# Performance work log

Hardware: AMD Instinct MI355X
Metric: run time of the kernel (lower is better)

Reference implementation:

```python
import jax, jax.numpy as jnp
import numpy as np

GRID_MIN = -2.0
GRID_MAX = 2.0
NUM_GRIDS = 8
IN_DIM = 512
OUT_DIM = 512
N = 16384
SPLINE_SCALE = 0.1


def setup_inputs() -> dict:
    key = jax.random.key(0)
    k_x, k_sw, k_w, k_b = jax.random.split(key, 4)
    x = jax.random.normal(k_x, (N, IN_DIM), dtype=jnp.float32)
    grid = jnp.linspace(GRID_MIN, GRID_MAX, NUM_GRIDS, dtype=jnp.float32)
    spline_weight = jax.random.normal(k_sw, (IN_DIM * NUM_GRIDS, OUT_DIM), dtype=jnp.float32) * SPLINE_SCALE
    bound = 1.0 / np.sqrt(IN_DIM)
    base_w = jax.random.uniform(k_w, (OUT_DIM, IN_DIM), minval=-bound, maxval=bound, dtype=jnp.float32)
    base_b = jax.random.uniform(k_b, (OUT_DIM,), minval=-bound, maxval=bound, dtype=jnp.float32)
    return {"x": x, "grid": grid, "spline_weight": spline_weight, "base_w": base_w, "base_b": base_b}


def reference(x, grid, spline_weight, base_w, base_b):
    # Gaussian RBF basis over the grid: (N, in_dim, num_grids)
    h = (GRID_MAX - GRID_MIN) / (NUM_GRIDS - 1)  # grid spacing
    basis = jnp.exp(-(((x[..., None] - grid) / h) ** 2))
    ret = basis.reshape(x.shape[0], -1) @ spline_weight  # (N, out_dim)
    base = jax.nn.silu(x) @ base_w.T + base_b
    return ret + base
```

## Files before the change

### kernel.cpp

```cpp
#include <hip/hip_runtime.h>
#include <hip/hip_bf16.h>

typedef __attribute__((ext_vector_type(8))) short short8;
typedef __attribute__((ext_vector_type(4))) float floatx4;

#define N_ROWS   16384
#define IN_DIM   512
#define OUT_DIM  512
#define K_SPLINE 4096
#define K_TOT    4608
#define NKT      72
#define NPER     36
#define NSPER    32
#define NKTILE   144
#define L2E      1.4426950408889634f
#define C2E      0.13533528323661270f

__device__ __forceinline__ unsigned short f2bf(float f) {
    unsigned int u = __float_as_uint(f);
    unsigned int r = u + 0x7FFFu + ((u >> 16) & 1u);
    return (unsigned short)(r >> 16);
}

__device__ __forceinline__ unsigned packtrunc(float f0, float f1) {
    return __builtin_amdgcn_perm(__float_as_uint(f1), __float_as_uint(f0), 0x07060302);
}

__global__ __launch_bounds__(256) void prep_kernel(
    const float* __restrict__ sw, const float* __restrict__ bw,
    unsigned short* __restrict__ Btf)
{
    const int t     = threadIdx.x;
    const int lane  = t & 63;
    const int kt32  = blockIdx.x * 4 + (t >> 6);
    const int ct    = blockIdx.y;
    const int mn    = lane & 15, q = lane >> 4;
    const int n     = ct * 16 + mn;
    const int kbase = kt32 * 32 + q * 8;
    short8 v;
    if (kbase < K_SPLINE) {
        #pragma unroll
        for (int j = 0; j < 8; ++j)
            v[j] = (short)f2bf(sw[(size_t)(kbase + j) * OUT_DIM + n]);
    } else {
        #pragma unroll
        for (int j = 0; j < 8; ++j)
            v[j] = (short)f2bf(bw[(size_t)n * IN_DIM + (kbase + j - K_SPLINE)]);
    }
    reinterpret_cast<short8*>(Btf)[(size_t)(ct * NKTILE + kt32) * 64 + lane] = v;
}

__device__ __forceinline__ uint4 basis_pack(float X) {
    const float u = fmaf(1.75f, X, 3.5f);
    float b = __builtin_amdgcn_exp2f(-(u * u) * L2E);
    float r = __builtin_amdgcn_exp2f(fmaf(2.0f * L2E, u, -L2E));
    float v[8];
    v[0] = b;
    #pragma unroll
    for (int j = 1; j < 8; ++j) { b *= r; r *= C2E; v[j] = b; }
    uint4 p;
    p.x = packtrunc(v[0], v[1]);
    p.y = packtrunc(v[2], v[3]);
    p.z = packtrunc(v[4], v[5]);
    p.w = packtrunc(v[6], v[7]);
    return p;
}

__device__ __forceinline__ void stageA128(unsigned short* dst, const float* xrow,
                                          int rowA, int colq, int p, float4 xsp)
{
    unsigned short* arow = dst + rowA * 128;
    if (p < NSPER) {
        const float xv[4] = {xsp.x, xsp.y, xsp.z, xsp.w};
        #pragma unroll
        for (int e = 0; e < 4; ++e) {
            const uint4 pk = basis_pack(xv[e]);
            const int blk = (colq * 4 + e) ^ (rowA & 15);
            *reinterpret_cast<uint4*>(arow + blk * 8) = pk;
        }
    } else {
        const float* xs = xrow + (p - NSPER) * 128 + colq * 32;
        #pragma unroll
        for (int e = 0; e < 4; ++e) {
            const float4 a0 = *reinterpret_cast<const float4*>(xs + e * 8);
            const float4 a1 = *reinterpret_cast<const float4*>(xs + e * 8 + 4);
            const float f[8] = {a0.x, a0.y, a0.z, a0.w, a1.x, a1.y, a1.z, a1.w};
            float s[8];
            #pragma unroll
            for (int j = 0; j < 8; ++j)
                s[j] = f[j] * __builtin_amdgcn_rcpf(
                    1.0f + __builtin_amdgcn_exp2f(-f[j] * L2E));
            uint4 pk;
            pk.x = packtrunc(s[0], s[1]);
            pk.y = packtrunc(s[2], s[3]);
            pk.z = packtrunc(s[4], s[5]);
            pk.w = packtrunc(s[6], s[7]);
            const int blk = (colq * 4 + e) ^ (rowA & 15);
            *reinterpret_cast<uint4*>(arow + blk * 8) = pk;
        }
    }
}

template<bool PREP>
__device__ __forceinline__ void load_bfrags(short8 dst[4][2], const short8* __restrict__ Bf,
                                            const size_t* bbase, int kt,
                                            const float* __restrict__ sw,
                                            const float* __restrict__ bw,
                                            int col0, int lane)
{
    if (kt >= NKT) return;
    if (PREP) {
        #pragma unroll
        for (int nt = 0; nt < 4; ++nt)
            #pragma unroll
            for (int s = 0; s < 2; ++s)
                dst[nt][s] = Bf[bbase[nt] + (size_t)(kt * 2 + s) * 64];
    } else {
        const int mn = lane & 15, q = lane >> 4;
        #pragma unroll
        for (int nt = 0; nt < 4; ++nt) {
            const int n = col0 + nt * 16 + mn;
            #pragma unroll
            for (int s = 0; s < 2; ++s) {
                short8 v;
                #pragma unroll
                for (int j = 0; j < 8; ++j) {
                    const int k = (kt * 2 + s) * 32 + q * 8 + j;
                    const float val = (k < K_SPLINE)
                        ? sw[(size_t)k * OUT_DIM + n]
                        : bw[(size_t)n * IN_DIM + (k - K_SPLINE)];
                    v[j] = (short)f2bf(val);
                }
                dst[nt][s] = v;
            }
        }
    }
}

template<bool PREP>
__global__ __launch_bounds__(256, 2) void kan_kernel(
    const float* __restrict__ x,
    const unsigned short* __restrict__ Btf,
    const float* __restrict__ sw,
    const float* __restrict__ bw,
    const float* __restrict__ bias,
    float* __restrict__ out)
{
    __shared__ unsigned short Als[2][64 * 128];

    const int tid  = threadIdx.x;
    const int wn   = tid >> 6;
    const int lane = tid & 63;
    const int q    = lane >> 4;
    const int mn   = lane & 15;
    const int bid  = blockIdx.x;
    const int row0 = (bid >> 1) * 64;
    const int col0 = (bid & 1) * 256 + wn * 64;

    const int rowA = tid >> 2;
    const int colq = tid & 3;
    const float* xrow = x + (size_t)(row0 + rowA) * IN_DIM;

    size_t bbase[4];
    #pragma unroll
    for (int nt = 0; nt < 4; ++nt)
        bbase[nt] = (size_t)(((col0 >> 4) + nt) * NKTILE) * 64 + lane;
    const short8* Bf = reinterpret_cast<const short8*>(Btf);

    floatx4 acc[4][4];
    #pragma unroll
    for (int i = 0; i < 4; ++i)
        #pragma unroll
        for (int j = 0; j < 4; ++j)
            acc[i][j] = (floatx4){0.f, 0.f, 0.f, 0.f};

    short8 bb[2][4][2];

    float4 xsp = *reinterpret_cast<const float4*>(xrow + colq * 4);
    stageA128(&Als[0][0], xrow, rowA, colq, 0, xsp);
    load_bfrags<PREP>(bb[0], Bf, bbase, 0, sw, bw, col0, lane);
    xsp = *reinterpret_cast<const float4*>(xrow + 16 + colq * 4);
    __syncthreads();

    for (int p = 0; p < NPER; ++p) {
        const unsigned short* Acur = &Als[p & 1][0];
        unsigned short*       Anxt = &Als[(p & 1) ^ 1][0];

        load_bfrags<PREP>(bb[1], Bf, bbase, 2 * p + 1, sw, bw, col0, lane);

        if (p + 1 < NPER) {
            stageA128(Anxt, xrow, rowA, colq, p + 1, xsp);
            if (p + 2 < NSPER)
                xsp = *reinterpret_cast<const float4*>(
                    xrow + (p + 2) * 16 + colq * 4);
        }

        #pragma unroll
        for (int hh = 0; hh < 2; ++hh) {
            #pragma unroll
            for (int s = 0; s < 2; ++s) {
                const int st = hh * 2 + s;
                short8 af[4];
                #pragma unroll
                for (int mt = 0; mt < 4; ++mt) {
                    const int r = mt * 16 + mn;
                    af[mt] = *reinterpret_cast<const short8*>(
                        Acur + r * 128 + (((st * 4 + q) ^ (r & 15)) * 8));
                }
                #pragma unroll
                for (int mt = 0; mt < 4; ++mt)
                    #pragma unroll
                    for (int nt = 0; nt < 4; ++nt)
                        acc[mt][nt] = __builtin_amdgcn_mfma_f32_16x16x32_bf16(
                            af[mt], bb[hh][nt][s], acc[mt][nt], 0, 0, 0);
            }
            if (hh == 0)
                load_bfrags<PREP>(bb[0], Bf, bbase, 2 * p + 2, sw, bw, col0, lane);
        }
        __syncthreads();
    }

    #pragma unroll
    for (int nt = 0; nt < 4; ++nt) {
        const int col = col0 + nt * 16 + mn;
        const float bv = bias[col];
        #pragma unroll
        for (int mt = 0; mt < 4; ++mt) {
            const int rb = row0 + mt * 16 + q * 4;
            #pragma unroll
            for (int e = 0; e < 4; ++e)
                out[(size_t)(rb + e) * OUT_DIM + col] = acc[mt][nt][e] + bv;
        }
    }
}

extern "C" void kernel_launch(void* const* d_in, const int* in_sizes, int n_in,
                              void* d_out, int out_size, void* d_ws, size_t ws_size,
                              hipStream_t stream)
{
    const float* x    = (const float*)d_in[0];
    const float* sw   = (const float*)d_in[2];
    const float* bw   = (const float*)d_in[3];
    const float* bias = (const float*)d_in[4];
    float* out = (float*)d_out;

    const size_t bt_bytes = (size_t)OUT_DIM * K_TOT * sizeof(unsigned short);
    if (ws_size >= bt_bytes) {
        unsigned short* Btf = (unsigned short*)d_ws;
        prep_kernel<<<dim3(NKTILE / 4, OUT_DIM / 16), 256, 0, stream>>>(sw, bw, Btf);
        kan_kernel<true><<<dim3(512), 256, 0, stream>>>(
            x, Btf, sw, bw, bias, out);
    } else {
        kan_kernel<false><<<dim3(512), 256, 0, stream>>>(
            x, nullptr, sw, bw, bias, out);
    }
}
```

Measured before the change: 167.1 us.

## Switch to 32x32x16 MFMA tiles with interleaved staging and software-pipelined A loads

```diff
diff --git a/kernel.cpp b/kernel.cpp
--- a/kernel.cpp
+++ b/kernel.cpp
@@ -1,18 +1,19 @@
 #include <hip/hip_runtime.h>
 #include <hip/hip_bf16.h>
 
-typedef __attribute__((ext_vector_type(8))) short short8;
-typedef __attribute__((ext_vector_type(4))) float floatx4;
+typedef __attribute__((ext_vector_type(8)))  short  short8;
+typedef __attribute__((ext_vector_type(16))) float  floatx16;
 
 #define N_ROWS   16384
 #define IN_DIM   512
 #define OUT_DIM  512
 #define K_SPLINE 4096
 #define K_TOT    4608
-#define NKT      72
+#define NKT16    288
+#define NKT64    72
 #define NPER     36
 #define NSPER    32
-#define NKTILE   144
+#define NCT      16
 #define L2E      1.4426950408889634f
 #define C2E      0.13533528323661270f
 
@@ -30,24 +31,23 @@
     const float* __restrict__ sw, const float* __restrict__ bw,
     unsigned short* __restrict__ Btf)
 {
-    const int t     = threadIdx.x;
-    const int lane  = t & 63;
-    const int kt32  = blockIdx.x * 4 + (t >> 6);
-    const int ct    = blockIdx.y;
-    const int mn    = lane & 15, q = lane >> 4;
-    const int n     = ct * 16 + mn;
-    const int kbase = kt32 * 32 + q * 8;
+    const int t    = threadIdx.x;
+    const int lane = t & 63;
+    const int kt16 = blockIdx.x * 4 + (t >> 6);
+    const int ct   = blockIdx.y;
+    const int n    = ct * 32 + (lane & 31);
+    const int kb   = kt16 * 16 + (lane >> 5) * 8;
     short8 v;
-    if (kbase < K_SPLINE) {
+    if (kb < K_SPLINE) {
         #pragma unroll
         for (int j = 0; j < 8; ++j)
-            v[j] = (short)f2bf(sw[(size_t)(kbase + j) * OUT_DIM + n]);
+            v[j] = (short)f2bf(sw[(size_t)(kb + j) * OUT_DIM + n]);
     } else {
         #pragma unroll
         for (int j = 0; j < 8; ++j)
-            v[j] = (short)f2bf(bw[(size_t)n * IN_DIM + (kbase + j - K_SPLINE)]);
-    }
-    reinterpret_cast<short8*>(Btf)[(size_t)(ct * NKTILE + kt32) * 64 + lane] = v;
+            v[j] = (short)f2bf(bw[(size_t)n * IN_DIM + (kb + j - K_SPLINE)]);
+    }
+    reinterpret_cast<short8*>(Btf)[(size_t)(ct * NKT16 + kt16) * 64 + lane] = v;
 }
 
 __device__ __forceinline__ uint4 basis_pack(float X) {
@@ -66,66 +66,58 @@
     return p;
 }
 
-__device__ __forceinline__ void stageA128(unsigned short* dst, const float* xrow,
-                                          int rowA, int colq, int p, float4 xsp)
-{
-    unsigned short* arow = dst + rowA * 128;
-    if (p < NSPER) {
-        const float xv[4] = {xsp.x, xsp.y, xsp.z, xsp.w};
-        #pragma unroll
-        for (int e = 0; e < 4; ++e) {
-            const uint4 pk = basis_pack(xv[e]);
-            const int blk = (colq * 4 + e) ^ (rowA & 15);
-            *reinterpret_cast<uint4*>(arow + blk * 8) = pk;
-        }
+__device__ __forceinline__ void stage_spl_e(unsigned short* arow, int rowA, int colq,
+                                            float X, int e)
+{
+    const uint4 pk = basis_pack(X);
+    const int blk = (colq * 4 + e) ^ (rowA & 15);
+    *reinterpret_cast<uint4*>(arow + blk * 8) = pk;
+}
+
+__device__ __forceinline__ void stage_silu_e(unsigned short* arow, const float* xs,
+                                             int rowA, int colq, int e)
+{
+    const float4 a0 = *reinterpret_cast<const float4*>(xs + e * 8);
+    const float4 a1 = *reinterpret_cast<const float4*>(xs + e * 8 + 4);
+    const float f[8] = {a0.x, a0.y, a0.z, a0.w, a1.x, a1.y, a1.z, a1.w};
+    float sv[8];
+    #pragma unroll
+    for (int j = 0; j < 8; ++j)
+        sv[j] = f[j] * __builtin_amdgcn_rcpf(
+            1.0f + __builtin_amdgcn_exp2f(-f[j] * L2E));
+    uint4 pk;
+    pk.x = packtrunc(sv[0], sv[1]);
+    pk.y = packtrunc(sv[2], sv[3]);
+    pk.z = packtrunc(sv[4], sv[5]);
+    pk.w = packtrunc(sv[6], sv[7]);
+    const int blk = (colq * 4 + e) ^ (rowA & 15);
+    *reinterpret_cast<uint4*>(arow + blk * 8) = pk;
+}
+
+template<bool PREP>
+__device__ __forceinline__ void load_bhalf(short8 dst[2][4], const short8* __restrict__ Bf,
+                                           const unsigned* boff, int kt64,
+                                           const float* __restrict__ sw,
+                                           const float* __restrict__ bw,
+                                           int col0, int lane)
+{
+    if (PREP) {
+        #pragma unroll
+        for (int nt = 0; nt < 2; ++nt)
+            #pragma unroll
+            for (int s = 0; s < 4; ++s)
+                dst[nt][s] = Bf[boff[nt] + (unsigned)(kt64 * 4 + s) * 64u];
     } else {
-        const float* xs = xrow + (p - NSPER) * 128 + colq * 32;
-        #pragma unroll
-        for (int e = 0; e < 4; ++e) {
-            const float4 a0 = *reinterpret_cast<const float4*>(xs + e * 8);
-            const float4 a1 = *reinterpret_cast<const float4*>(xs + e * 8 + 4);
-            const float f[8] = {a0.x, a0.y, a0.z, a0.w, a1.x, a1.y, a1.z, a1.w};
-            float s[8];
-            #pragma unroll
-            for (int j = 0; j < 8; ++j)
-                s[j] = f[j] * __builtin_amdgcn_rcpf(
-                    1.0f + __builtin_amdgcn_exp2f(-f[j] * L2E));
-            uint4 pk;
-            pk.x = packtrunc(s[0], s[1]);
-            pk.y = packtrunc(s[2], s[3]);
-            pk.z = packtrunc(s[4], s[5]);
-            pk.w = packtrunc(s[6], s[7]);
-            const int blk = (colq * 4 + e) ^ (rowA & 15);
-            *reinterpret_cast<uint4*>(arow + blk * 8) = pk;
-        }
-    }
-}
-
-template<bool PREP>
-__device__ __forceinline__ void load_bfrags(short8 dst[4][2], const short8* __restrict__ Bf,
-                                            const size_t* bbase, int kt,
-                                            const float* __restrict__ sw,
-                                            const float* __restrict__ bw,
-                                            int col0, int lane)
-{
-    if (kt >= NKT) return;
-    if (PREP) {
-        #pragma unroll
-        for (int nt = 0; nt < 4; ++nt)
-            #pragma unroll
-            for (int s = 0; s < 2; ++s)
-                dst[nt][s] = Bf[bbase[nt] + (size_t)(kt * 2 + s) * 64];
-    } else {
-        const int mn = lane & 15, q = lane >> 4;
-        #pragma unroll
-        for (int nt = 0; nt < 4; ++nt) {
-            const int n = col0 + nt * 16 + mn;
-            #pragma unroll
-            for (int s = 0; s < 2; ++s) {
+        #pragma unroll
+        for (int nt = 0; nt < 2; ++nt) {
+            const int n = col0 + nt * 32 + (lane & 31);
+            #pragma unroll
+            for (int s = 0; s < 4; ++s) {
+                const int kb = (kt64 * 4 + s) * 16 + (lane >> 5) * 8;
                 short8 v;
                 #pragma unroll
                 for (int j = 0; j < 8; ++j) {
-                    const int k = (kt * 2 + s) * 32 + q * 8 + j;
+                    const int k = kb + j;
                     const float val = (k < K_SPLINE)
                         ? sw[(size_t)k * OUT_DIM + n]
                         : bw[(size_t)n * IN_DIM + (k - K_SPLINE)];
@@ -135,6 +127,58 @@
             }
         }
     }
+}
+
+template<int MODE, bool PREP>
+__device__ __forceinline__ void period_body(
+    int p,
+    const unsigned short* __restrict__ Acur,
+    unsigned short* __restrict__ anrow,
+    short8 bb[2][2][4], floatx16 acc[2][2],
+    const int aoff[2][8],
+    const unsigned* boff, const short8* __restrict__ Bf,
+    float4& xsp, const float* __restrict__ xrow, int rowA, int colq,
+    const float* __restrict__ sw, const float* __restrict__ bw,
+    int col0, int lane)
+{
+    const float xv[4] = {xsp.x, xsp.y, xsp.z, xsp.w};
+    const float* xs = (MODE == 1) ? (xrow + (p + 1 - NSPER) * 128 + colq * 32)
+                                  : xrow;
+
+    short8 af[2][2];
+    #pragma unroll
+    for (int mt = 0; mt < 2; ++mt)
+        af[0][mt] = *reinterpret_cast<const short8*>(Acur + aoff[mt][0]);
+
+    #pragma unroll
+    for (int st = 0; st < 8; ++st) {
+        const int hh = st >> 2, s = st & 3, cb = st & 1;
+        if (st < 7) {
+            #pragma unroll
+            for (int mt = 0; mt < 2; ++mt)
+                af[cb ^ 1][mt] = *reinterpret_cast<const short8*>(
+                    Acur + aoff[mt][st + 1]);
+        }
+        if (MODE == 0 && st < 4) stage_spl_e(anrow, rowA, colq, xv[st], st);
+        if (MODE == 1 && st < 4) stage_silu_e(anrow, xs, rowA, colq, st);
+        if (st == 0)
+            load_bhalf<PREP>(bb[1], Bf, boff, 2 * p + 1, sw, bw, col0, lane);
+        if (MODE != 2 && st == 4)
+            load_bhalf<PREP>(bb[0], Bf, boff, 2 * p + 2, sw, bw, col0, lane);
+        if (MODE == 0 && st == 3) {
+            const int pp = (p + 2 < NSPER) ? p + 2 : NSPER - 1;
+            xsp = *reinterpret_cast<const float4*>(xrow + pp * 16 + colq * 4);
+        }
+        __builtin_amdgcn_s_setprio(1);
+        #pragma unroll
+        for (int mt = 0; mt < 2; ++mt)
+            #pragma unroll
+            for (int nt = 0; nt < 2; ++nt)
+                acc[mt][nt] = __builtin_amdgcn_mfma_f32_32x32x16_bf16(
+                    af[cb][mt], bb[hh][nt][s], acc[mt][nt], 0, 0, 0);
+        __builtin_amdgcn_s_setprio(0);
+    }
+    __syncthreads();
 }
 
 template<bool PREP>
@@ -151,8 +195,8 @@
     const int tid  = threadIdx.x;
     const int wn   = tid >> 6;
     const int lane = tid & 63;
-    const int q    = lane >> 4;
-    const int mn   = lane & 15;
+    const int h    = lane >> 5;
+    const int mn   = lane & 31;
     const int bid  = blockIdx.x;
     const int row0 = (bid >> 1) * 64;
     const int col0 = (bid & 1) * 256 + wn * 64;
@@ -161,75 +205,72 @@
     const int colq = tid & 3;
     const float* xrow = x + (size_t)(row0 + rowA) * IN_DIM;
 
-    size_t bbase[4];
-    #pragma unroll
-    for (int nt = 0; nt < 4; ++nt)
-        bbase[nt] = (size_t)(((col0 >> 4) + nt) * NKTILE) * 64 + lane;
+    unsigned boff[2];
+    #pragma unroll
+    for (int nt = 0; nt < 2; ++nt)
+        boff[nt] = (unsigned)(((col0 >> 5) + nt) * NKT16) * 64u + (unsigned)lane;
     const short8* Bf = reinterpret_cast<const short8*>(Btf);
 
-    floatx4 acc[4][4];
-    #pragma unroll
-    for (int i = 0; i < 4; ++i)
-        #pragma unroll
-        for (int j = 0; j < 4; ++j)
-            acc[i][j] = (floatx4){0.f, 0.f, 0.f, 0.f};
-
-    short8 bb[2][4][2];
+    int aoff[2][8];
+    #pragma unroll
+    for (int mt = 0; mt < 2; ++mt) {
+        const int r = mt * 32 + mn;
+        #pragma unroll
+        for (int st = 0; st < 8; ++st)
+            aoff[mt][st] = r * 128 + (((st * 2 + h) ^ (r & 15)) * 8);
+    }
+
+    floatx16 acc[2][2];
+    #pragma unroll
+    for (int i = 0; i < 2; ++i)
+        #pragma unroll
+        for (int j = 0; j < 2; ++j)
+            #pragma unroll
+            for (int e = 0; e < 16; ++e)
+                acc[i][j][e] = 0.f;
+
+    short8 bb[2][2][4];
 
     float4 xsp = *reinterpret_cast<const float4*>(xrow + colq * 4);
-    stageA128(&Als[0][0], xrow, rowA, colq, 0, xsp);
-    load_bfrags<PREP>(bb[0], Bf, bbase, 0, sw, bw, col0, lane);
+    {
+        unsigned short* arow0 = &Als[0][0] + rowA * 128;
+        const float xv0[4] = {xsp.x, xsp.y, xsp.z, xsp.w};
+        #pragma unroll
+        for (int e = 0; e < 4; ++e)
+            stage_spl_e(arow0, rowA, colq, xv0[e], e);
+    }
+    load_bhalf<PREP>(bb[0], Bf, boff, 0, sw, bw, col0, lane);
     xsp = *reinterpret_cast<const float4*>(xrow + 16 + colq * 4);
     __syncthreads();
 
-    for (int p = 0; p < NPER; ++p) {
-        const unsigned short* Acur = &Als[p & 1][0];
-        unsigned short*       Anxt = &Als[(p & 1) ^ 1][0];
-
-        load_bfrags<PREP>(bb[1], Bf, bbase, 2 * p + 1, sw, bw, col0, lane);
-
-        if (p + 1 < NPER) {
-            stageA128(Anxt, xrow, rowA, colq, p + 1, xsp);
-            if (p + 2 < NSPER)
-                xsp = *reinterpret_cast<const float4*>(
-                    xrow + (p + 2) * 16 + colq * 4);
-        }
-
-        #pragma unroll
-        for (int hh = 0; hh < 2; ++hh) {
-            #pragma unroll
-            for (int s = 0; s < 2; ++s) {
-                const int st = hh * 2 + s;
-                short8 af[4];
-                #pragma unroll
-                for (int mt = 0; mt < 4; ++mt) {
-                    const int r = mt * 16 + mn;
-                    af[mt] = *reinterpret_cast<const short8*>(
-                        Acur + r * 128 + (((st * 4 + q) ^ (r & 15)) * 8));
-                }
-                #pragma unroll
-                for (int mt = 0; mt < 4; ++mt)
-                    #pragma unroll
-                    for (int nt = 0; nt < 4; ++nt)
-                        acc[mt][nt] = __builtin_amdgcn_mfma_f32_16x16x32_bf16(
-                            af[mt], bb[hh][nt][s], acc[mt][nt], 0, 0, 0);
+    #pragma unroll 1
+    for (int p = 0; p < NSPER - 1; ++p)
+        period_body<0, PREP>(p, &Als[p & 1][0],
+                             &Als[(p & 1) ^ 1][0] + rowA * 128,
+                             bb, acc, aoff, boff, Bf, xsp, xrow, rowA, colq,
+                             sw, bw, col0, lane);
+    #pragma unroll 1
+    for (int p = NSPER - 1; p < NPER - 1; ++p)
+        period_body<1, PREP>(p, &Als[p & 1][0],
+                             &Als[(p & 1) ^ 1][0] + rowA * 128,
+                             bb, acc, aoff, boff, Bf, xsp, xrow, rowA, colq,
+                             sw, bw, col0, lane);
+    period_body<2, PREP>(NPER - 1, &Als[(NPER - 1) & 1][0],
+                         &Als[0][0] + rowA * 128,
+                         bb, acc, aoff, boff, Bf, xsp, xrow, rowA, colq,
+                         sw, bw, col0, lane);
+
+    #pragma unroll
+    for (int nt = 0; nt < 2; ++nt) {
+        const int col = col0 + nt * 32 + mn;
+        const float bv = bias[col];
+        #pragma unroll
+        for (int mt = 0; mt < 2; ++mt) {
+            #pragma unroll
+            for (int e = 0; e < 16; ++e) {
+                const int row = row0 + mt * 32 + (e & 3) + 8 * (e >> 2) + 4 * h;
+                out[(size_t)row * OUT_DIM + col] = acc[mt][nt][e] + bv;
             }
-            if (hh == 0)
-                load_bfrags<PREP>(bb[0], Bf, bbase, 2 * p + 2, sw, bw, col0, lane);
-        }
-        __syncthreads();
-    }
-
-    #pragma unroll
-    for (int nt = 0; nt < 4; ++nt) {
-        const int col = col0 + nt * 16 + mn;
-        const float bv = bias[col];
-        #pragma unroll
-        for (int mt = 0; mt < 4; ++mt) {
-            const int rb = row0 + mt * 16 + q * 4;
-            #pragma unroll
-            for (int e = 0; e < 4; ++e)
-                out[(size_t)(rb + e) * OUT_DIM + col] = acc[mt][nt][e] + bv;
         }
     }
 }
@@ -247,7 +288,7 @@
     const size_t bt_bytes = (size_t)OUT_DIM * K_TOT * sizeof(unsigned short);
     if (ws_size >= bt_bytes) {
         unsigned short* Btf = (unsigned short*)d_ws;
-        prep_kernel<<<dim3(NKTILE / 4, OUT_DIM / 16), 256, 0, stream>>>(sw, bw, Btf);
+        prep_kernel<<<dim3(NKT16 / 4, NCT), 256, 0, stream>>>(sw, bw, Btf);
         kan_kernel<true><<<dim3(512), 256, 0, stream>>>(
             x, Btf, sw, bw, bias, out);
     } else {
```

Result: slower. 174.9 us (+4.7%).
